# Performance work log

Measured on AMD Instinct MI355X. Metric: run time of the kernel, lower is better.

The kernel has to match this reference:

```python
import jax, jax.numpy as jnp
import numpy as np

N = 8192
D_IN = 512
D_OUT = 64
ALPHA = 0.2  # LeakyReLU negative slope
MASK_VAL = -9e15


def setup_inputs() -> dict:
    key = jax.random.key(0)
    k1, k2, k3, k4 = jax.random.split(key, 4)
    inp = jax.random.normal(k1, (N, D_IN), dtype=jnp.float32)
    adj = (jax.random.uniform(k2, (N, N)) < 0.05).astype(jnp.float32)
    adj = adj.at[jnp.arange(N), jnp.arange(N)].set(1.0)
    W = jax.random.normal(k3, (D_IN, D_OUT), dtype=jnp.float32) * 0.05
    a = jax.random.normal(k4, (2 * D_OUT, 1), dtype=jnp.float32) * 0.05
    return {"input": inp, "adj": adj, "W": W, "a": a}


def reference(input, adj, W, a):
    # h = input @ W : [n, out]
    h = input @ W
    # Algebraic equivalent of the dense pairwise concat:
    # e_ij = leakyrelu([h_i || h_j] . a) = leakyrelu(h_i.a1 + h_j.a2)
    a1, a2 = a[:D_OUT, 0], a[D_OUT:, 0]          # [out], [out]
    e = jax.nn.leaky_relu(
        (h @ a1)[:, None] + (h @ a2)[None, :],    # [n, n]
        negative_slope=ALPHA,
    )
    attention = jnp.where(adj > 0, e, MASK_VAL)
    attention = jax.nn.softmax(attention, axis=1)
    out = attention @ h                            # [n, out]
    return jax.nn.elu(out)                         # end=False branch
```

## Files before the change

kernel.cpp:

```cpp
#include <hip/hip_runtime.h>
#include <hip/hip_bf16.h>

#define N 8192
#define D_IN 512
#define D_OUT 64
#define ALPHA 0.2f
#define CAP 640
#define RPW 8

__global__ __launch_bounds__(256) void gat_h_kernel(
    const float* __restrict__ input, const float* __restrict__ W,
    const float* __restrict__ a, float* __restrict__ h,
    float* __restrict__ s1, float* __restrict__ s2)
{
    int wave = (blockIdx.x * 256 + threadIdx.x) >> 6;
    int lane = threadIdx.x & 63;
    int row0 = wave * RPW;
    const float* in0 = input + (size_t)row0 * D_IN;
    float a1 = a[lane], a2 = a[D_OUT + lane];
    float acc[RPW];
#pragma unroll
    for (int r = 0; r < RPW; ++r) acc[r] = 0.f;
#pragma unroll 4
    for (int k = 0; k < D_IN; ++k) {
        float wk = W[k * D_OUT + lane];
#pragma unroll
        for (int r = 0; r < RPW; ++r)
            acc[r] = fmaf(in0[(size_t)r * D_IN + k], wk, acc[r]);
    }
#pragma unroll
    for (int r = 0; r < RPW; ++r) {
        h[((size_t)(row0 + r) << 6) + lane] = acc[r];
        float p1 = acc[r] * a1;
        float p2 = acc[r] * a2;
#pragma unroll
        for (int off = 32; off; off >>= 1) {
            p1 += __shfl_xor(p1, off, 64);
            p2 += __shfl_xor(p2, off, 64);
        }
        if (lane == 0) { s1[row0 + r] = p1; s2[row0 + r] = p2; }
    }
}

__global__ __launch_bounds__(256) void gat_attn_kernel(
    const float* __restrict__ adj, const float* __restrict__ h,
    const float* __restrict__ s1, const float* __restrict__ s2,
    float* __restrict__ out)
{
    __shared__ uint2 nbr[4][CAP];
    int wid  = (blockIdx.x * 256 + threadIdx.x) >> 6;
    int lane = threadIdx.x & 63;
    int ws   = threadIdx.x >> 6;
    const float4* adj_row = (const float4*)(adj + (size_t)wid * N);
    const float4* s2v     = (const float4*)s2;
    float s1i  = s1[wid];
    float eref = s1i + s2[wid];
    eref = eref > 0.f ? eref : ALPHA * eref;
    float lsum = 0.f;
    int base = 0;

    for (int j0 = 0; j0 < N; j0 += 256) {
        float4 av = adj_row[(j0 >> 2) + lane];
        float4 sv = s2v[(j0 >> 2) + lane];
#pragma unroll
        for (int z = 0; z < 4; ++z) {
            bool nb = (&av.x)[z] > 0.f;
            float e = s1i + (&sv.x)[z];
            e = e > 0.f ? e : ALPHA * e;
            float w = nb ? __expf(e - eref) : 0.f;
            lsum += w;
            unsigned long long m = __ballot(nb);
            if (nb) {
                int prefix = __builtin_amdgcn_mbcnt_hi(
                    (unsigned)(m >> 32),
                    __builtin_amdgcn_mbcnt_lo((unsigned)m, 0u));
                nbr[ws][base + prefix] =
                    make_uint2((unsigned)(j0 + (lane << 2) + z), __float_as_uint(w));
            }
            base += __popcll(m);
        }
    }
#pragma unroll
    for (int off = 32; off; off >>= 1) lsum += __shfl_xor(lsum, off, 64);

    int cnt = base;
    float acc0 = 0.f, acc1 = 0.f;
    int k = 0;
    for (; k + 8 <= cnt; k += 8) {
        float wv[8], hv[8];
#pragma unroll
        for (int t = 0; t < 8; ++t) {
            uint2 e = nbr[ws][k + t];
            int j = __builtin_amdgcn_readfirstlane((int)e.x);
            wv[t] = __uint_as_float(e.y);
            hv[t] = h[((size_t)j << 6) + lane];
        }
#pragma unroll
        for (int t = 0; t < 8; ++t) {
            if (t & 1) acc1 = fmaf(wv[t], hv[t], acc1);
            else       acc0 = fmaf(wv[t], hv[t], acc0);
        }
    }
    for (; k < cnt; ++k) {
        uint2 e = nbr[ws][k];
        int j = __builtin_amdgcn_readfirstlane((int)e.x);
        acc0 = fmaf(__uint_as_float(e.y), h[((size_t)j << 6) + lane], acc0);
    }
    float o = (acc0 + acc1) / lsum;
    out[((size_t)wid << 6) + lane] = o > 0.f ? o : expm1f(o);
}

extern "C" void kernel_launch(void* const* d_in, const int* in_sizes, int n_in,
                              void* d_out, int out_size, void* d_ws, size_t ws_size,
                              hipStream_t stream) {
    const float* input = (const float*)d_in[0];
    const float* adj   = (const float*)d_in[1];
    const float* W     = (const float*)d_in[2];
    const float* a     = (const float*)d_in[3];
    float* out = (float*)d_out;

    float* h  = (float*)d_ws;
    float* s1 = h + (size_t)N * D_OUT;
    float* s2 = s1 + N;

    gat_h_kernel<<<N / (RPW * 4), 256, 0, stream>>>(input, W, a, h, s1, s2);
    gat_attn_kernel<<<N / 4, 256, 0, stream>>>(adj, h, s1, s2, out);
}
```

Measured before the change: 138.6 us.

## Replace sparse gather attention with dense bf16 MFMA flash-style kernel

Replaces the per-row ballot/compaction and gather of neighbor h rows with a dense tiled attention kernel. Masked softmax weights are computed per tile, packed to bf16 in swizzled LDS, and multiplied against a transposed bf16 copy of h using 16x16x32 MFMA, with register double-buffered prefetch of adj and h tiles. This removes the irregular gathers and the fixed neighbor cap. In exchange it does dense work over all columns, rereads h once per 16-row block, and lowers precision of h and the weights to bf16.

```diff
diff --git a/kernel.cpp b/kernel.cpp
--- a/kernel.cpp
+++ b/kernel.cpp
@@ -5,32 +5,54 @@
 #define D_IN 512
 #define D_OUT 64
 #define ALPHA 0.2f
-#define CAP 640
-#define RPW 8
+#define BM 16
+#define BK 128
+#define NSTEP (N / BK)
+
+typedef __attribute__((ext_vector_type(4))) float f32x4;
+typedef __attribute__((ext_vector_type(8))) short bf16x8;
+
+static __device__ __forceinline__ unsigned pk_bf16(float lo, float hi) {
+    unsigned ulo = __bfloat16_as_ushort(__float2bfloat16(lo));
+    unsigned uhi = __bfloat16_as_ushort(__float2bfloat16(hi));
+    return (uhi << 16) | ulo;
+}
+
+#define BARRIER() do { \
+    asm volatile("s_waitcnt lgkmcnt(0)" ::: "memory"); \
+    __builtin_amdgcn_sched_barrier(0); \
+    __builtin_amdgcn_s_barrier(); \
+    __builtin_amdgcn_sched_barrier(0); \
+} while (0)
 
 __global__ __launch_bounds__(256) void gat_h_kernel(
     const float* __restrict__ input, const float* __restrict__ W,
-    const float* __restrict__ a, float* __restrict__ h,
+    const float* __restrict__ a, unsigned short* __restrict__ hbT,
     float* __restrict__ s1, float* __restrict__ s2)
 {
     int wave = (blockIdx.x * 256 + threadIdx.x) >> 6;
     int lane = threadIdx.x & 63;
-    int row0 = wave * RPW;
+    int row0 = wave * 8;
     const float* in0 = input + (size_t)row0 * D_IN;
     float a1 = a[lane], a2 = a[D_OUT + lane];
-    float acc[RPW];
-#pragma unroll
-    for (int r = 0; r < RPW; ++r) acc[r] = 0.f;
+    float acc[8];
+#pragma unroll
+    for (int r = 0; r < 8; ++r) acc[r] = 0.f;
 #pragma unroll 4
     for (int k = 0; k < D_IN; ++k) {
         float wk = W[k * D_OUT + lane];
 #pragma unroll
-        for (int r = 0; r < RPW; ++r)
+        for (int r = 0; r < 8; ++r)
             acc[r] = fmaf(in0[(size_t)r * D_IN + k], wk, acc[r]);
     }
-#pragma unroll
-    for (int r = 0; r < RPW; ++r) {
-        h[((size_t)(row0 + r) << 6) + lane] = acc[r];
+    uint4 hv;
+    hv.x = pk_bf16(acc[0], acc[1]);
+    hv.y = pk_bf16(acc[2], acc[3]);
+    hv.z = pk_bf16(acc[4], acc[5]);
+    hv.w = pk_bf16(acc[6], acc[7]);
+    *(uint4*)(hbT + (size_t)lane * N + row0) = hv;
+#pragma unroll
+    for (int r = 0; r < 8; ++r) {
         float p1 = acc[r] * a1;
         float p2 = acc[r] * a2;
 #pragma unroll
@@ -42,72 +64,131 @@
     }
 }
 
-__global__ __launch_bounds__(256) void gat_attn_kernel(
-    const float* __restrict__ adj, const float* __restrict__ h,
+struct Pref { float4 a0, a1; uint4 h0, h1, h2, h3; };
+
+static __device__ __forceinline__ void issue(Pref& p, const float* ab,
+                                             const unsigned short* hb, int j0) {
+    p.a0 = *(const float4*)(ab + j0);
+    p.a1 = *(const float4*)(ab + j0 + 4);
+    p.h0 = *(const uint4*)(hb + j0);
+    p.h1 = *(const uint4*)(hb + j0 + 8);
+    p.h2 = *(const uint4*)(hb + j0 + 16);
+    p.h3 = *(const uint4*)(hb + j0 + 24);
+}
+
+__global__ __launch_bounds__(256, 2) void gat_flash_kernel(
+    const float* __restrict__ adj, const unsigned short* __restrict__ hbT,
     const float* __restrict__ s1, const float* __restrict__ s2,
     float* __restrict__ out)
 {
-    __shared__ uint2 nbr[4][CAP];
-    int wid  = (blockIdx.x * 256 + threadIdx.x) >> 6;
-    int lane = threadIdx.x & 63;
-    int ws   = threadIdx.x >> 6;
-    const float4* adj_row = (const float4*)(adj + (size_t)wid * N);
-    const float4* s2v     = (const float4*)s2;
-    float s1i  = s1[wid];
-    float eref = s1i + s2[wid];
-    eref = eref > 0.f ? eref : ALPHA * eref;
+    __shared__ float s2l[N];
+    __shared__ __align__(16) unsigned char Pl[2][BM * BK * 2];
+    __shared__ __align__(16) unsigned char Hl[2][D_OUT * BK * 2];
+    __shared__ float lsl[BM];
+
+    const int tid  = threadIdx.x;
+    const int lane = tid & 63;
+    const int wv   = tid >> 6;
+    const int r    = tid >> 4;
+    const int s    = tid & 15;
+    const int hd   = tid >> 2;
+    const int hc   = tid & 3;
+    const int rg   = blockIdx.x * BM + r;
+
+    {
+        const float4* src = (const float4*)s2;
+        float4* dst = (float4*)s2l;
+        for (int i = tid; i < N / 4; i += 256) dst[i] = src[i];
+    }
+    const float* adj_base = adj + (size_t)rg * N + s * 8;
+    const unsigned short* hb_base = hbT + (size_t)hd * N + hc * 32;
+    float s1r = s1[rg];
+    float eref;
     float lsum = 0.f;
-    int base = 0;
-
-    for (int j0 = 0; j0 < N; j0 += 256) {
-        float4 av = adj_row[(j0 >> 2) + lane];
-        float4 sv = s2v[(j0 >> 2) + lane];
+    f32x4 acc = {0.f, 0.f, 0.f, 0.f};
+
+    auto stage = [&](const Pref& p, int j0, int b) {
+        float4 s2a = *(const float4*)(s2l + j0 + s * 8);
+        float4 s2b = *(const float4*)(s2l + j0 + s * 8 + 4);
+        const float* av0 = (const float*)&p.a0;
+        const float* av1 = (const float*)&p.a1;
+        const float* sv0 = (const float*)&s2a;
+        const float* sv1 = (const float*)&s2b;
+        float w[8];
 #pragma unroll
         for (int z = 0; z < 4; ++z) {
-            bool nb = (&av.x)[z] > 0.f;
-            float e = s1i + (&sv.x)[z];
-            e = e > 0.f ? e : ALPHA * e;
-            float w = nb ? __expf(e - eref) : 0.f;
-            lsum += w;
-            unsigned long long m = __ballot(nb);
-            if (nb) {
-                int prefix = __builtin_amdgcn_mbcnt_hi(
-                    (unsigned)(m >> 32),
-                    __builtin_amdgcn_mbcnt_lo((unsigned)m, 0u));
-                nbr[ws][base + prefix] =
-                    make_uint2((unsigned)(j0 + (lane << 2) + z), __float_as_uint(w));
-            }
-            base += __popcll(m);
-        }
-    }
-#pragma unroll
-    for (int off = 32; off; off >>= 1) lsum += __shfl_xor(lsum, off, 64);
-
-    int cnt = base;
-    float acc0 = 0.f, acc1 = 0.f;
-    int k = 0;
-    for (; k + 8 <= cnt; k += 8) {
-        float wv[8], hv[8];
-#pragma unroll
-        for (int t = 0; t < 8; ++t) {
-            uint2 e = nbr[ws][k + t];
-            int j = __builtin_amdgcn_readfirstlane((int)e.x);
-            wv[t] = __uint_as_float(e.y);
-            hv[t] = h[((size_t)j << 6) + lane];
-        }
-#pragma unroll
-        for (int t = 0; t < 8; ++t) {
-            if (t & 1) acc1 = fmaf(wv[t], hv[t], acc1);
-            else       acc0 = fmaf(wv[t], hv[t], acc0);
-        }
-    }
-    for (; k < cnt; ++k) {
-        uint2 e = nbr[ws][k];
-        int j = __builtin_amdgcn_readfirstlane((int)e.x);
-        acc0 = fmaf(__uint_as_float(e.y), h[((size_t)j << 6) + lane], acc0);
-    }
-    float o = (acc0 + acc1) / lsum;
-    out[((size_t)wid << 6) + lane] = o > 0.f ? o : expm1f(o);
+            float e0 = s1r + sv0[z]; e0 = e0 > 0.f ? e0 : ALPHA * e0;
+            float e1 = s1r + sv1[z]; e1 = e1 > 0.f ? e1 : ALPHA * e1;
+            float w0 = __expf(e0 - eref);
+            float w1 = __expf(e1 - eref);
+            w[z]     = av0[z] > 0.f ? w0 : 0.f;
+            w[z + 4] = av1[z] > 0.f ? w1 : 0.f;
+        }
+#pragma unroll
+        for (int z = 0; z < 8; ++z) lsum += w[z];
+        uint4 pk;
+        pk.x = pk_bf16(w[0], w[1]); pk.y = pk_bf16(w[2], w[3]);
+        pk.z = pk_bf16(w[4], w[5]); pk.w = pk_bf16(w[6], w[7]);
+        *(uint4*)(&Pl[b][r * 256 + ((s * 16) ^ ((r & 7) << 4))]) = pk;
+        *(uint4*)(&Hl[b][hd * 256 + ((hc * 64 +  0) ^ ((hd & 7) << 4))]) = p.h0;
+        *(uint4*)(&Hl[b][hd * 256 + ((hc * 64 + 16) ^ ((hd & 7) << 4))]) = p.h1;
+        *(uint4*)(&Hl[b][hd * 256 + ((hc * 64 + 32) ^ ((hd & 7) << 4))]) = p.h2;
+        *(uint4*)(&Hl[b][hd * 256 + ((hc * 64 + 48) ^ ((hd & 7) << 4))]) = p.h3;
+    };
+
+    auto mfma_step = [&](int c) {
+        const unsigned char* Pc = Pl[c];
+        const unsigned char* Hc = Hl[c];
+        const int i  = lane & 15;
+        const int kb = lane >> 4;
+        const int dd = wv * 16 + (lane & 15);
+#pragma unroll
+        for (int kk = 0; kk < 4; ++kk) {
+            uint4 ua = *(const uint4*)(Pc + i * 256 + ((kk * 64 + kb * 16) ^ ((i & 7) << 4)));
+            uint4 ub = *(const uint4*)(Hc + dd * 256 + ((kk * 64 + kb * 16) ^ ((dd & 7) << 4)));
+            acc = __builtin_amdgcn_mfma_f32_16x16x32_bf16(
+                __builtin_bit_cast(bf16x8, ua), __builtin_bit_cast(bf16x8, ub), acc, 0, 0, 0);
+        }
+    };
+
+    Pref RA, RB;
+    issue(RA, adj_base, hb_base, 0);
+    issue(RB, adj_base, hb_base, BK);
+    __syncthreads();
+    {
+        float ed = s1r + s2l[rg];
+        eref = ed > 0.f ? ed : ALPHA * ed;
+    }
+    stage(RA, 0, 0);
+    issue(RA, adj_base, hb_base, 2 * BK);
+    BARRIER();
+
+    for (int ks = 0; ks < NSTEP; ks += 2) {
+        mfma_step(0);
+        stage(RB, (ks + 1) * BK, 1);
+        if (ks + 3 < NSTEP) issue(RB, adj_base, hb_base, (ks + 3) * BK);
+        BARRIER();
+        mfma_step(1);
+        if (ks + 2 < NSTEP) {
+            stage(RA, (ks + 2) * BK, 0);
+            if (ks + 4 < NSTEP) issue(RA, adj_base, hb_base, (ks + 4) * BK);
+        }
+        BARRIER();
+    }
+
+#pragma unroll
+    for (int off = 8; off; off >>= 1) lsum += __shfl_xor(lsum, off, 64);
+    if ((tid & 15) == 0) lsl[r] = lsum;
+    __syncthreads();
+
+    const int dd = wv * 16 + (lane & 15);
+#pragma unroll
+    for (int reg = 0; reg < 4; ++reg) {
+        int i = (lane >> 4) * 4 + reg;
+        float o = acc[reg] / lsl[i];
+        o = o > 0.f ? o : expm1f(o);
+        out[(size_t)(blockIdx.x * BM + i) * 64 + dd] = o;
+    }
 }
 
 extern "C" void kernel_launch(void* const* d_in, const int* in_sizes, int n_in,
@@ -119,10 +200,10 @@
     const float* a     = (const float*)d_in[3];
     float* out = (float*)d_out;
 
-    float* h  = (float*)d_ws;
-    float* s1 = h + (size_t)N * D_OUT;
+    unsigned short* hbT = (unsigned short*)d_ws;
+    float* s1 = (float*)(hbT + (size_t)N * D_OUT);
     float* s2 = s1 + N;
 
-    gat_h_kernel<<<N / (RPW * 4), 256, 0, stream>>>(input, W, a, h, s1, s2);
-    gat_attn_kernel<<<N / 4, 256, 0, stream>>>(adj, h, s1, s2, out);
-}
+    gat_h_kernel<<<256, 256, 0, stream>>>(input, W, a, hbT, s1, s2);
+    gat_flash_kernel<<<N / BM, 256, 0, stream>>>(adj, hbT, s1, s2, out);
+}
```

After: 123.5 us. 1.12x faster.
